# Kernel optimization log

Measured on AMD Instinct MI355X. Metric: run time of the kernel, lower is better.

The kernel has to match this reference:

```python
import jax, jax.numpy as jnp
import numpy as np

B, N, DIN, DOUT, H, DH, DC, NL, L = 8, 256, 64, 64, 8, 8, 64, 32, 2
SCALE = DH ** -0.5  # out_dim-per-head scaling used by both attention variants


def _ln(x, g, b):
    m = jnp.mean(x, -1, keepdims=True)
    v = jnp.mean((x - m) ** 2, -1, keepdims=True)
    return (x - m) * jax.lax.rsqrt(v + 1e-5) * g + b


def _cross_attn(x, ctx, mask_b, wq, wkv, wo, bo):
    # CrossAttentionLayer: standard softmax attention with clamp(-5,5)
    b, n, _ = x.shape
    m = ctx.shape[1]
    q = (x @ wq).reshape(b, n, H, DH).transpose(0, 2, 1, 3)
    k, v = jnp.split(ctx @ wkv, 2, axis=-1)
    k = k.reshape(b, m, H, DH).transpose(0, 2, 1, 3)
    v = v.reshape(b, m, H, DH).transpose(0, 2, 1, 3)
    sim = jnp.einsum('bhid,bhjd->bhij', q, k) * SCALE
    if mask_b is not None:
        sim = jnp.where(mask_b[:, None, None, :], sim, -jnp.finfo(sim.dtype).max)
    sim = jnp.clip(sim, -5.0, 5.0)
    attn = jax.nn.softmax(sim, axis=-1)
    out = jnp.einsum('bhij,bhjd->bhid', attn, v)
    out = out.transpose(0, 2, 1, 3).reshape(b, n, H * DH)
    return out @ wo + bo


def _mha_edge(p, e, k_RW, mask, wq, wk, we, wv):
    # GraphiT MultiHeadAttentionLayer with edge features + k_RW attention PE
    Q = (p @ wq).reshape(B, N, H, DH)
    K = (p @ wk).reshape(B, N, H, DH) * SCALE
    V = (p @ wv).reshape(B, N, H, DH).transpose(0, 2, 1, 3)  # [B,H,N,d]
    E = (e @ we).reshape(B, N, N, H, DH)
    scores = jnp.einsum('bihk,bjhk,bijhk->bhij', Q, K, E)
    scores = jnp.exp(scores - jnp.max(scores, axis=(-2, -1), keepdims=True))
    scores = scores * mask[:, None, :, None] * mask[:, None, None, :]
    scores = scores * k_RW
    denom = jnp.clip(jnp.sum(scores, -1, keepdims=True), 1e-6, None)
    out = jnp.einsum('bhij,bhjd->bhid', scores, V) / denom
    return out.transpose(0, 2, 1, 3).reshape(B, N, H * DH)


def setup_inputs() -> dict:
    key = jax.random.key(0)
    ks = jax.random.split(key, 32)
    rn = lambda k, s: jax.random.normal(k, s, dtype=jnp.float32)
    inp = {
        'h': rn(ks[0], (B, N, DIN)),
        'p': rn(ks[1], (B, N, DIN)),
        'e': rn(ks[2], (B, N, N, DIN)),
        'k_RW': jax.random.uniform(ks[3], (B, 1, N, N), dtype=jnp.float32),
        'queries': rn(ks[4], (B, NL, DC)),
        'mask': jnp.ones((B, N), dtype=jnp.float32),
        # attention_p (MultiHeadAttentionLayer) weights
        'wq_p': rn(ks[5], (DIN, H * DH)) * 0.05,
        'wk_p': rn(ks[6], (DIN, H * DH)) * 0.05,
        'we_p': rn(ks[7], (DIN, H * DH)) * 0.05,
        'wv_p': rn(ks[8], (DIN, H * DH)) * 0.05,
        'wo_p': rn(ks[9], (DOUT, DOUT)) * 0.05,
        # cross_attention_h (queries attend to nodes)
        'cq_wq': rn(ks[10], (DC, H * DH)) * 0.05,
        'cq_wkv': rn(ks[11], (DIN, 2 * H * DH)) * 0.05,
        'cq_wo': rn(ks[12], (H * DH, DC)) * 0.05,
        'cq_bo': jnp.zeros((DC,), dtype=jnp.float32),
        # L_cross latent self-attention layers (stacked)
        'sa_wq': rn(ks[13], (L, DC, H * DH)) * 0.05,
        'sa_wkv': rn(ks[14], (L, DC, 2 * H * DH)) * 0.05,
        'sa_wo': rn(ks[15], (L, H * DH, DC)) * 0.05,
        'sa_bo': jnp.zeros((L, DC), dtype=jnp.float32),
        # O_queries, norms, FFN
        'oq_w': rn(ks[16], (DC, DC)) * 0.05,
        'ln1_g': jnp.ones((DC,), dtype=jnp.float32),
        'ln1_b': jnp.zeros((DC,), dtype=jnp.float32),
        'ffn_w1': rn(ks[17], (DC, 2 * DC)) * 0.05,
        'ffn_w2': rn(ks[18], (2 * DC, DC)) * 0.05,
        'ln2_g': jnp.ones((DC,), dtype=jnp.float32),
        'ln2_b': jnp.zeros((DC,), dtype=jnp.float32),
    }
    return inp


def reference(h, p, e, k_RW, queries, mask,
              wq_p, wk_p, we_p, wv_p, wo_p,
              cq_wq, cq_wkv, cq_wo, cq_bo,
              sa_wq, sa_wkv, sa_wo, sa_bo,
              oq_w, ln1_g, ln1_b, ffn_w1, ffn_w2, ln2_g, ln2_b):
    # forward_p: update positional encoding via edge-modulated attention
    p_attn = _mha_edge(p, e, k_RW, mask, wq_p, wk_p, we_p, wv_p)
    p_new = p + jnp.tanh(p_attn @ wo_p)  # residual, no dropout (eval)
    # combine node features with updated PE (use_node_pe='sum')
    h_c = h + p_new
    mask_b = mask > 0.5
    # perceiver cross-attention: latents attend to nodes
    q = queries + _cross_attn(queries, h_c, mask_b, cq_wq, cq_wkv, cq_wo, cq_bo)
    # L_cross latent self-attention blocks with residual
    for i in range(L):
        q = q + _cross_attn(q, q, None, sa_wq[i], sa_wkv[i], sa_wo[i], sa_bo[i])
    # O_queries projection + layer norm
    q = _ln(q @ oq_w, ln1_g, ln1_b)
    # feed-forward block on queries
    ff = jax.nn.relu(q @ ffn_w1) @ ffn_w2
    q = _ln(q + ff, ln2_g, ln2_b)
    return q
```

## Files before the change

kernel.cpp:

```cpp
#include <hip/hip_runtime.h>
#include <hip/hip_bf16.h>
#include <math.h>

typedef __bf16 bf16x8 __attribute__((ext_vector_type(8)));
typedef float floatx4 __attribute__((ext_vector_type(4)));

#define ATT_SCALE 0.35355339059327373f

__device__ __forceinline__ __bf16 f2b(float x) { return (__bf16)x; }

__global__ void k_proj(const float* __restrict__ p, const float* __restrict__ quer,
                       const float* __restrict__ wq, const float* __restrict__ wk,
                       const float* __restrict__ wv, const float* __restrict__ cq_wq,
                       float* __restrict__ Q, float* __restrict__ Ks,
                       float* __restrict__ V, float* __restrict__ q1) {
  int blk = blockIdx.x, t = threadIdx.x;
  __shared__ float xr[64];
  if (blk < 2048) {
    xr[t] = p[blk * 64 + t];
    __syncthreads();
    float aq = 0.f, ak = 0.f, av = 0.f;
    for (int c = 0; c < 64; c++) {
      float x = xr[c];
      aq += x * wq[c * 64 + t];
      ak += x * wk[c * 64 + t];
      av += x * wv[c * 64 + t];
    }
    Q[blk * 64 + t] = aq;
    Ks[blk * 64 + t] = ak * ATT_SCALE;
    V[blk * 64 + t] = av;
  } else {
    int r = blk - 2048;
    xr[t] = quer[r * 64 + t];
    __syncthreads();
    float a = 0.f;
    for (int c = 0; c < 64; c++) a += xr[c] * cq_wq[c * 64 + t];
    q1[r * 64 + t] = a;
  }
}

__global__ __launch_bounds__(256) void k_edge(
    const float* __restrict__ e, const float* __restrict__ we,
    const float* __restrict__ krw, const float* __restrict__ mask,
    const float* __restrict__ hin, const float* __restrict__ pin,
    const float* __restrict__ wo, const float* __restrict__ cq_wkv,
    const float* __restrict__ Q, const float* __restrict__ Ks,
    const float* __restrict__ V, float* __restrict__ Kc, float* __restrict__ Vc) {
  int bi = blockIdx.x;
  int b = bi >> 8;
  int t = threadIdx.x;
  int w = t >> 6, l = t & 63;
  int l15 = l & 15, quad = l >> 4, half8 = (l >> 3) & 1, d = l & 7;

  bf16x8 wfrag[4][2];
  for (int nt = 0; nt < 4; nt++)
    for (int kc = 0; kc < 2; kc++)
      for (int jj = 0; jj < 8; jj++)
        wfrag[nt][kc][jj] = f2b(we[(kc * 32 + quad * 8 + jj) * 64 + nt * 16 + l15]);

  float qv[4];
  for (int nt = 0; nt < 4; nt++) qv[nt] = Q[bi * 64 + nt * 16 + l15];
  float mi = mask[bi];

  float aout[4] = {0.f, 0.f, 0.f, 0.f};
  float aden[4] = {0.f, 0.f, 0.f, 0.f};

  for (int mt = 0; mt < 4; mt++) {
    int j0 = w * 64 + mt * 16;
    const float* ep = e + ((long)bi * 256 + j0 + l15) * 64 + quad * 8;
    float4 ea = *reinterpret_cast<const float4*>(ep);
    float4 eb4 = *reinterpret_cast<const float4*>(ep + 4);
    float4 ec = *reinterpret_cast<const float4*>(ep + 32);
    float4 ed4 = *reinterpret_cast<const float4*>(ep + 36);
    bf16x8 a0, a1;
    a0[0] = f2b(ea.x); a0[1] = f2b(ea.y); a0[2] = f2b(ea.z); a0[3] = f2b(ea.w);
    a0[4] = f2b(eb4.x); a0[5] = f2b(eb4.y); a0[6] = f2b(eb4.z); a0[7] = f2b(eb4.w);
    a1[0] = f2b(ec.x); a1[1] = f2b(ec.y); a1[2] = f2b(ec.z); a1[3] = f2b(ec.w);
    a1[4] = f2b(ed4.x); a1[5] = f2b(ed4.y); a1[6] = f2b(ed4.z); a1[7] = f2b(ed4.w);

    int jr0 = j0 + quad * 4;
    float krw_r[4], mj_r[4];
    for (int r = 0; r < 4; r++) {
      krw_r[r] = krw[(long)bi * 256 + jr0 + r];
      mj_r[r] = mask[b * 256 + jr0 + r];
    }
    for (int nt = 0; nt < 4; nt++) {
      floatx4 acc = {0.f, 0.f, 0.f, 0.f};
      acc = __builtin_amdgcn_mfma_f32_16x16x32_bf16(a0, wfrag[nt][0], acc, 0, 0, 0);
      acc = __builtin_amdgcn_mfma_f32_16x16x32_bf16(a1, wfrag[nt][1], acc, 0, 0, 0);
      int hk = nt * 16 + l15;
      int hbase = hk & 56;
      for (int r = 0; r < 4; r++) {
        int jr = jr0 + r;
        float s = acc[r] * qv[nt] * Ks[(b * 256 + jr) * 64 + hk];
        s += __shfl_xor(s, 1);
        s += __shfl_xor(s, 2);
        s += __shfl_xor(s, 4);
        float wg = __expf(s) * krw_r[r] * mj_r[r];
        aden[nt] += wg;
        aout[nt] += wg * V[(b * 256 + jr) * 64 + hbase + d];
      }
    }
  }
  for (int nt = 0; nt < 4; nt++) {
    float o = aout[nt], dn = aden[nt];
    o += __shfl_xor(o, 16); o += __shfl_xor(o, 32);
    dn += __shfl_xor(dn, 16); dn += __shfl_xor(dn, 32);
    aout[nt] = o; aden[nt] = dn;
  }

  __shared__ float red[4][64];
  __shared__ float redden[4][8];
  __shared__ float pav[64];
  __shared__ float hcl[64];
  if (l < 16) {
    for (int nt = 0; nt < 4; nt++) {
      int head = nt * 2 + half8;
      red[w][head * 8 + d] = aout[nt];
      if (d == 0) redden[w][head] = aden[nt];
    }
  }
  __syncthreads();
  if (t < 64) {
    int head = t >> 3;
    float num = red[0][t] + red[1][t] + red[2][t] + red[3][t];
    float den = redden[0][head] + redden[1][head] + redden[2][head] + redden[3][head];
    num *= mi;
    den = fmaxf(den * mi, 1e-6f);
    pav[t] = num / den;
  }
  __syncthreads();
  if (t < 64) {
    float a = 0.f;
    for (int c = 0; c < 64; c++) a += pav[c] * wo[c * 64 + t];
    hcl[t] = hin[bi * 64 + t] + pin[bi * 64 + t] + tanhf(a);
  }
  __syncthreads();
  if (t < 128) {
    float a = 0.f;
    for (int c = 0; c < 64; c++) a += hcl[c] * cq_wkv[c * 128 + t];
    if (t < 64) Kc[bi * 64 + t] = a;
    else        Vc[bi * 64 + t - 64] = a;
  }
}

__global__ void k_cross(const float* __restrict__ q1, const float* __restrict__ Kc,
                        const float* __restrict__ Vc, const float* __restrict__ mask,
                        float* __restrict__ oc) {
  int bh = blockIdx.x, b = bh >> 3, h = bh & 7;
  int t = threadIdx.x, r = t >> 3, g = t & 7;
  __shared__ float qL[32][8];
  qL[r][g] = q1[(b * 32 + r) * 64 + h * 8 + g];
  __syncthreads();
  float num[8] = {0.f, 0.f, 0.f, 0.f, 0.f, 0.f, 0.f, 0.f};
  float den = 0.f;
  for (int jj = 0; jj < 32; jj++) {
    int j = jj * 8 + g;
    const float* kp = Kc + (b * 256 + j) * 64 + h * 8;
    float s = 0.f;
    for (int dd = 0; dd < 8; dd++) s += qL[r][dd] * kp[dd];
    s *= ATT_SCALE;
    float mj = mask[b * 256 + j];
    s = (mj > 0.5f) ? s : -1e30f;
    s = fminf(fmaxf(s, -5.f), 5.f);
    float ex = __expf(s);
    den += ex;
    const float* vp = Vc + (b * 256 + j) * 64 + h * 8;
    for (int dd = 0; dd < 8; dd++) num[dd] += ex * vp[dd];
  }
  den += __shfl_xor(den, 1); den += __shfl_xor(den, 2); den += __shfl_xor(den, 4);
  for (int dd = 0; dd < 8; dd++) {
    float v = num[dd];
    v += __shfl_xor(v, 1); v += __shfl_xor(v, 2); v += __shfl_xor(v, 4);
    num[dd] = v;
  }
  oc[(b * 32 + r) * 64 + h * 8 + g] = num[g] / den;
}

__global__ void k_projqkv(const float* __restrict__ attn_in, const float* __restrict__ Wo,
                          const float* __restrict__ bo, const float* __restrict__ residp,
                          const float* __restrict__ wql, const float* __restrict__ wkvl,
                          float* __restrict__ q_out, float* __restrict__ qq,
                          float* __restrict__ kvb) {
  int r = blockIdx.x, t = threadIdx.x;
  __shared__ float oL[64];
  __shared__ float qL[64];
  oL[t] = attn_in[r * 64 + t];
  __syncthreads();
  float a = 0.f;
  for (int c = 0; c < 64; c++) a += oL[c] * Wo[c * 64 + t];
  float qvv = residp[r * 64 + t] + a + bo[t];
  q_out[r * 64 + t] = qvv;
  qL[t] = qvv;
  __syncthreads();
  float aq = 0.f, ak = 0.f, av = 0.f;
  for (int c = 0; c < 64; c++) {
    float x = qL[c];
    aq += x * wql[c * 64 + t];
    ak += x * wkvl[c * 128 + t];
    av += x * wkvl[c * 128 + 64 + t];
  }
  qq[r * 64 + t] = aq;
  kvb[r * 128 + t] = ak;
  kvb[r * 128 + 64 + t] = av;
}

__global__ void k_sattn(const float* __restrict__ qq, const float* __restrict__ kvb,
                        float* __restrict__ os) {
  int bh = blockIdx.x, b = bh >> 3, h = bh & 7;
  int t = threadIdx.x, r = t >> 3, g = t & 7;
  __shared__ float qL[32][8];
  qL[r][g] = qq[(b * 32 + r) * 64 + h * 8 + g];
  __syncthreads();
  float num[8] = {0.f, 0.f, 0.f, 0.f, 0.f, 0.f, 0.f, 0.f};
  float den = 0.f;
  for (int jj = 0; jj < 4; jj++) {
    int j = jj * 8 + g;
    const float* kp = kvb + (b * 32 + j) * 128 + h * 8;
    float s = 0.f;
    for (int dd = 0; dd < 8; dd++) s += qL[r][dd] * kp[dd];
    s *= ATT_SCALE;
    s = fminf(fmaxf(s, -5.f), 5.f);
    float ex = __expf(s);
    den += ex;
    for (int dd = 0; dd < 8; dd++) num[dd] += ex * kp[64 + dd];
  }
  den += __shfl_xor(den, 1); den += __shfl_xor(den, 2); den += __shfl_xor(den, 4);
  for (int dd = 0; dd < 8; dd++) {
    float v = num[dd];
    v += __shfl_xor(v, 1); v += __shfl_xor(v, 2); v += __shfl_xor(v, 4);
    num[dd] = v;
  }
  os[(b * 32 + r) * 64 + h * 8 + g] = num[g] / den;
}

__global__ void k_final(const float* __restrict__ os, const float* __restrict__ Wo,
                        const float* __restrict__ bo, const float* __restrict__ qprev,
                        const float* __restrict__ oqw, const float* __restrict__ g1,
                        const float* __restrict__ b1, const float* __restrict__ w1,
                        const float* __restrict__ w2, const float* __restrict__ g2,
                        const float* __restrict__ b2v, float* __restrict__ out) {
  int r = blockIdx.x, t = threadIdx.x;
  __shared__ float oL[64];
  __shared__ float q2L[64];
  __shared__ float yL[64];
  __shared__ float hhs[128];
  oL[t] = os[r * 64 + t];
  __syncthreads();
  float a = 0.f;
  for (int c = 0; c < 64; c++) a += oL[c] * Wo[c * 64 + t];
  float q2 = qprev[r * 64 + t] + a + bo[t];
  q2L[t] = q2;
  __syncthreads();
  float x = 0.f;
  for (int c = 0; c < 64; c++) x += q2L[c] * oqw[c * 64 + t];
  float m = x;
  for (int off = 1; off < 64; off <<= 1) m += __shfl_xor(m, off);
  m *= (1.f / 64.f);
  float dv = x - m, vv = dv * dv;
  for (int off = 1; off < 64; off <<= 1) vv += __shfl_xor(vv, off);
  vv *= (1.f / 64.f);
  float y = dv * rsqrtf(vv + 1e-5f) * g1[t] + b1[t];
  yL[t] = y;
  __syncthreads();
  float h1 = 0.f, h2 = 0.f;
  for (int c = 0; c < 64; c++) {
    float xx = yL[c];
    h1 += xx * w1[c * 128 + t];
    h2 += xx * w1[c * 128 + 64 + t];
  }
  hhs[t] = fmaxf(h1, 0.f);
  hhs[t + 64] = fmaxf(h2, 0.f);
  __syncthreads();
  float ff = 0.f;
  for (int c = 0; c < 128; c++) ff += hhs[c] * w2[c * 64 + t];
  float z = y + ff;
  float m2 = z;
  for (int off = 1; off < 64; off <<= 1) m2 += __shfl_xor(m2, off);
  m2 *= (1.f / 64.f);
  float dz = z - m2, v2 = dz * dz;
  for (int off = 1; off < 64; off <<= 1) v2 += __shfl_xor(v2, off);
  v2 *= (1.f / 64.f);
  float z2 = dz * rsqrtf(v2 + 1e-5f) * g2[t] + b2v[t];
  out[r * 64 + t] = z2;
}

extern "C" void kernel_launch(void* const* d_in, const int* in_sizes, int n_in,
                              void* d_out, int out_size, void* d_ws, size_t ws_size,
                              hipStream_t stream) {
  const float* h_in   = (const float*)d_in[0];
  const float* p_in   = (const float*)d_in[1];
  const float* e_in   = (const float*)d_in[2];
  const float* krw    = (const float*)d_in[3];
  const float* quer   = (const float*)d_in[4];
  const float* mask   = (const float*)d_in[5];
  const float* wq_p   = (const float*)d_in[6];
  const float* wk_p   = (const float*)d_in[7];
  const float* we_p   = (const float*)d_in[8];
  const float* wv_p   = (const float*)d_in[9];
  const float* wo_p   = (const float*)d_in[10];
  const float* cq_wq  = (const float*)d_in[11];
  const float* cq_wkv = (const float*)d_in[12];
  const float* cq_wo  = (const float*)d_in[13];
  const float* cq_bo  = (const float*)d_in[14];
  const float* sa_wq  = (const float*)d_in[15];
  const float* sa_wkv = (const float*)d_in[16];
  const float* sa_wo  = (const float*)d_in[17];
  const float* sa_bo  = (const float*)d_in[18];
  const float* oq_w   = (const float*)d_in[19];
  const float* ln1_g  = (const float*)d_in[20];
  const float* ln1_b  = (const float*)d_in[21];
  const float* ffn_w1 = (const float*)d_in[22];
  const float* ffn_w2 = (const float*)d_in[23];
  const float* ln2_g  = (const float*)d_in[24];
  const float* ln2_b  = (const float*)d_in[25];

  float* ws = (float*)d_ws;
  float* Q   = ws;
  float* Ks  = Q + 131072;
  float* V   = Ks + 131072;
  float* q1  = V + 131072;
  float* Kc  = q1 + 16384;
  float* Vc  = Kc + 131072;
  float* oc  = Vc + 131072;
  float* q0  = oc + 16384;
  float* qq  = q0 + 16384;
  float* kvb = qq + 16384;
  float* osa = kvb + 32768;
  float* qc1 = osa + 16384;

  k_proj<<<2304, 64, 0, stream>>>(p_in, quer, wq_p, wk_p, wv_p, cq_wq, Q, Ks, V, q1);
  k_edge<<<2048, 256, 0, stream>>>(e_in, we_p, krw, mask, h_in, p_in, wo_p, cq_wkv,
                                   Q, Ks, V, Kc, Vc);
  k_cross<<<64, 256, 0, stream>>>(q1, Kc, Vc, mask, oc);
  k_projqkv<<<256, 64, 0, stream>>>(oc, cq_wo, cq_bo, quer,
                                    sa_wq, sa_wkv, q0, qq, kvb);
  k_sattn<<<64, 256, 0, stream>>>(qq, kvb, osa);
  k_projqkv<<<256, 64, 0, stream>>>(osa, sa_wo, sa_bo, q0,
                                    sa_wq + 4096, sa_wkv + 8192, qc1, qq, kvb);
  k_sattn<<<64, 256, 0, stream>>>(qq, kvb, osa);
  k_final<<<256, 64, 0, stream>>>(osa, sa_wo + 4096, sa_bo + 64, qc1, oq_w,
                                  ln1_g, ln1_b, ffn_w1, ffn_w2, ln2_g, ln2_b,
                                  (float*)d_out);
}
```

Baseline: 311.2 us.

## Transpose edge MFMA layout, prefetch edge tiles, fuse latent attention stages

The edge kernel swaps the MFMA operand order so each lane holds four head-dim outputs for a single key j. The per-row score reduction becomes one shuffle plus vector loads of Ks, V and Q, and the next edge tile is prefetched in registers. The downstream latent pipeline fuses cross-attention, output projection and next QKV projection into single kernels: k_crossf, k_sattnf, and k_finalf with K/V staged in LDS. This removes three kernel launches and intermediate round trips. The cost is more register pressure in k_edge and fewer, heavier blocks in the fused tail kernels.

Result: slower. 322.1 us (+3.5%).

```diff
diff --git a/kernel.cpp b/kernel.cpp
--- a/kernel.cpp
+++ b/kernel.cpp
@@ -50,7 +50,9 @@
   int b = bi >> 8;
   int t = threadIdx.x;
   int w = t >> 6, l = t & 63;
-  int l15 = l & 15, quad = l >> 4, half8 = (l >> 3) & 1, d = l & 7;
+  int l15 = l & 15, quad = l >> 4;
+  int hsel = quad >> 1;
+  int par = quad & 1;
 
   bf16x8 wfrag[4][2];
   for (int nt = 0; nt < 4; nt++)
@@ -58,66 +60,90 @@
       for (int jj = 0; jj < 8; jj++)
         wfrag[nt][kc][jj] = f2b(we[(kc * 32 + quad * 8 + jj) * 64 + nt * 16 + l15]);
 
-  float qv[4];
-  for (int nt = 0; nt < 4; nt++) qv[nt] = Q[bi * 64 + nt * 16 + l15];
+  float4 qv[4];
+#pragma unroll
+  for (int nt = 0; nt < 4; nt++)
+    qv[nt] = *(const float4*)(Q + bi * 64 + nt * 16 + quad * 4);
+
   float mi = mask[bi];
 
-  float aout[4] = {0.f, 0.f, 0.f, 0.f};
+  float aout[4][4];
   float aden[4] = {0.f, 0.f, 0.f, 0.f};
-
-  for (int mt = 0; mt < 4; mt++) {
-    int j0 = w * 64 + mt * 16;
-    const float* ep = e + ((long)bi * 256 + j0 + l15) * 64 + quad * 8;
-    float4 ea = *reinterpret_cast<const float4*>(ep);
-    float4 eb4 = *reinterpret_cast<const float4*>(ep + 4);
-    float4 ec = *reinterpret_cast<const float4*>(ep + 32);
-    float4 ed4 = *reinterpret_cast<const float4*>(ep + 36);
+#pragma unroll
+  for (int nt = 0; nt < 4; nt++)
+#pragma unroll
+    for (int d = 0; d < 4; d++) aout[nt][d] = 0.f;
+
+  const float* ebase = e + ((long)bi * 256 + w * 64 + l15) * 64 + quad * 8;
+  float4 c0 = *(const float4*)(ebase);
+  float4 c1 = *(const float4*)(ebase + 4);
+  float4 c2 = *(const float4*)(ebase + 32);
+  float4 c3 = *(const float4*)(ebase + 36);
+
+  for (int jt = 0; jt < 4; jt++) {
+    float4 n0, n1, n2, n3;
+    if (jt < 3) {
+      const float* np = ebase + (jt + 1) * 1024;
+      n0 = *(const float4*)(np);
+      n1 = *(const float4*)(np + 4);
+      n2 = *(const float4*)(np + 32);
+      n3 = *(const float4*)(np + 36);
+    }
+    int j = w * 64 + jt * 16 + l15;
     bf16x8 a0, a1;
-    a0[0] = f2b(ea.x); a0[1] = f2b(ea.y); a0[2] = f2b(ea.z); a0[3] = f2b(ea.w);
-    a0[4] = f2b(eb4.x); a0[5] = f2b(eb4.y); a0[6] = f2b(eb4.z); a0[7] = f2b(eb4.w);
-    a1[0] = f2b(ec.x); a1[1] = f2b(ec.y); a1[2] = f2b(ec.z); a1[3] = f2b(ec.w);
-    a1[4] = f2b(ed4.x); a1[5] = f2b(ed4.y); a1[6] = f2b(ed4.z); a1[7] = f2b(ed4.w);
-
-    int jr0 = j0 + quad * 4;
-    float krw_r[4], mj_r[4];
-    for (int r = 0; r < 4; r++) {
-      krw_r[r] = krw[(long)bi * 256 + jr0 + r];
-      mj_r[r] = mask[b * 256 + jr0 + r];
-    }
+    a0[0] = f2b(c0.x); a0[1] = f2b(c0.y); a0[2] = f2b(c0.z); a0[3] = f2b(c0.w);
+    a0[4] = f2b(c1.x); a0[5] = f2b(c1.y); a0[6] = f2b(c1.z); a0[7] = f2b(c1.w);
+    a1[0] = f2b(c2.x); a1[1] = f2b(c2.y); a1[2] = f2b(c2.z); a1[3] = f2b(c2.w);
+    a1[4] = f2b(c3.x); a1[5] = f2b(c3.y); a1[6] = f2b(c3.z); a1[7] = f2b(c3.w);
+
+    float kwm = krw[(long)bi * 256 + j] * mask[b * 256 + j];
+    const float* ksrow = Ks + ((long)(b * 256 + j)) * 64 + quad * 4;
+    const float* vrow = V + ((long)(b * 256 + j)) * 64 + hsel * 8 + par * 4;
+
+#pragma unroll
     for (int nt = 0; nt < 4; nt++) {
       floatx4 acc = {0.f, 0.f, 0.f, 0.f};
-      acc = __builtin_amdgcn_mfma_f32_16x16x32_bf16(a0, wfrag[nt][0], acc, 0, 0, 0);
-      acc = __builtin_amdgcn_mfma_f32_16x16x32_bf16(a1, wfrag[nt][1], acc, 0, 0, 0);
-      int hk = nt * 16 + l15;
-      int hbase = hk & 56;
-      for (int r = 0; r < 4; r++) {
-        int jr = jr0 + r;
-        float s = acc[r] * qv[nt] * Ks[(b * 256 + jr) * 64 + hk];
-        s += __shfl_xor(s, 1);
-        s += __shfl_xor(s, 2);
-        s += __shfl_xor(s, 4);
-        float wg = __expf(s) * krw_r[r] * mj_r[r];
-        aden[nt] += wg;
-        aout[nt] += wg * V[(b * 256 + jr) * 64 + hbase + d];
-      }
-    }
-  }
+      acc = __builtin_amdgcn_mfma_f32_16x16x32_bf16(wfrag[nt][0], a0, acc, 0, 0, 0);
+      acc = __builtin_amdgcn_mfma_f32_16x16x32_bf16(wfrag[nt][1], a1, acc, 0, 0, 0);
+      float4 kf = *(const float4*)(ksrow + nt * 16);
+      float s = acc[0] * kf.x * qv[nt].x + acc[1] * kf.y * qv[nt].y +
+                acc[2] * kf.z * qv[nt].z + acc[3] * kf.w * qv[nt].w;
+      s += __shfl_xor(s, 16);
+      float wg = __expf(s) * kwm;
+      aden[nt] += wg;
+      float4 va = *(const float4*)(vrow + nt * 16);
+      aout[nt][0] += wg * va.x; aout[nt][1] += wg * va.y;
+      aout[nt][2] += wg * va.z; aout[nt][3] += wg * va.w;
+    }
+    if (jt < 3) { c0 = n0; c1 = n1; c2 = n2; c3 = n3; }
+  }
+
+#pragma unroll
   for (int nt = 0; nt < 4; nt++) {
-    float o = aout[nt], dn = aden[nt];
-    o += __shfl_xor(o, 16); o += __shfl_xor(o, 32);
-    dn += __shfl_xor(dn, 16); dn += __shfl_xor(dn, 32);
-    aout[nt] = o; aden[nt] = dn;
+    float dn = aden[nt];
+    dn += __shfl_xor(dn, 1); dn += __shfl_xor(dn, 2);
+    dn += __shfl_xor(dn, 4); dn += __shfl_xor(dn, 8);
+    aden[nt] = dn;
+#pragma unroll
+    for (int d = 0; d < 4; d++) {
+      float o = aout[nt][d];
+      o += __shfl_xor(o, 1); o += __shfl_xor(o, 2);
+      o += __shfl_xor(o, 4); o += __shfl_xor(o, 8);
+      aout[nt][d] = o;
+    }
   }
 
   __shared__ float red[4][64];
   __shared__ float redden[4][8];
   __shared__ float pav[64];
   __shared__ float hcl[64];
-  if (l < 16) {
+  if (l15 == 0) {
+#pragma unroll
     for (int nt = 0; nt < 4; nt++) {
-      int head = nt * 2 + half8;
-      red[w][head * 8 + d] = aout[nt];
-      if (d == 0) redden[w][head] = aden[nt];
+      int head = nt * 2 + hsel;
+#pragma unroll
+      for (int d = 0; d < 4; d++) red[w][head * 8 + par * 4 + d] = aout[nt][d];
+      if (par == 0) redden[w][head] = aden[nt];
     }
   }
   __syncthreads();
@@ -144,145 +170,255 @@
   }
 }
 
-__global__ void k_cross(const float* __restrict__ q1, const float* __restrict__ Kc,
-                        const float* __restrict__ Vc, const float* __restrict__ mask,
-                        float* __restrict__ oc) {
-  int bh = blockIdx.x, b = bh >> 3, h = bh & 7;
-  int t = threadIdx.x, r = t >> 3, g = t & 7;
-  __shared__ float qL[32][8];
-  qL[r][g] = q1[(b * 32 + r) * 64 + h * 8 + g];
+__global__ __launch_bounds__(256) void k_crossf(
+    const float* __restrict__ q1, const float* __restrict__ Kc,
+    const float* __restrict__ Vc, const float* __restrict__ mask,
+    const float* __restrict__ quer, const float* __restrict__ cq_wo,
+    const float* __restrict__ cq_bo, const float* __restrict__ wq0,
+    const float* __restrict__ wkv0, float* __restrict__ q0g,
+    float* __restrict__ qqg, float* __restrict__ kvg) {
+  int blk = blockIdx.x, b = blk >> 3, rg = blk & 7;
+  int t = threadIdx.x, rr = t >> 6, l = t & 63, h = l >> 3, g = l & 7;
+  int gr = b * 32 + rg * 4 + rr;
+  __shared__ float ocs[4][64];
+  __shared__ float q0s[4][64];
+
+  {
+    const float* qp = q1 + gr * 64 + h * 8;
+    float4 qa = *(const float4*)qp, qb = *(const float4*)(qp + 4);
+    float num[8] = {0.f, 0.f, 0.f, 0.f, 0.f, 0.f, 0.f, 0.f};
+    float den = 0.f;
+#pragma unroll 4
+    for (int jj = 0; jj < 32; jj++) {
+      int j = jj * 8 + g;
+      const float* kp = Kc + (b * 256 + j) * 64 + h * 8;
+      float4 ka = *(const float4*)kp, kb = *(const float4*)(kp + 4);
+      float s = qa.x * ka.x + qa.y * ka.y + qa.z * ka.z + qa.w * ka.w +
+                qb.x * kb.x + qb.y * kb.y + qb.z * kb.z + qb.w * kb.w;
+      s *= ATT_SCALE;
+      float mj = mask[b * 256 + j];
+      s = (mj > 0.5f) ? s : -1e30f;
+      s = fminf(fmaxf(s, -5.f), 5.f);
+      float ex = __expf(s);
+      den += ex;
+      const float* vp = Vc + (b * 256 + j) * 64 + h * 8;
+      float4 va = *(const float4*)vp, vb = *(const float4*)(vp + 4);
+      num[0] += ex * va.x; num[1] += ex * va.y;
+      num[2] += ex * va.z; num[3] += ex * va.w;
+      num[4] += ex * vb.x; num[5] += ex * vb.y;
+      num[6] += ex * vb.z; num[7] += ex * vb.w;
+    }
+    den += __shfl_xor(den, 1); den += __shfl_xor(den, 2); den += __shfl_xor(den, 4);
+#pragma unroll
+    for (int d = 0; d < 8; d++) {
+      float v = num[d];
+      v += __shfl_xor(v, 1); v += __shfl_xor(v, 2); v += __shfl_xor(v, 4);
+      num[d] = v;
+    }
+    float sel = num[0];
+#pragma unroll
+    for (int d = 1; d < 8; d++) sel = (g == d) ? num[d] : sel;
+    ocs[rr][h * 8 + g] = sel / den;
+  }
+
+  int c = l;
+  {
+    float acc = quer[gr * 64 + c] + cq_bo[c];
+    for (int k = 0; k < 64; k++) acc += ocs[rr][k] * cq_wo[k * 64 + c];
+    q0g[gr * 64 + c] = acc;
+    q0s[rr][c] = acc;
+  }
+  {
+    float aq = 0.f, ak = 0.f, av = 0.f;
+    for (int k = 0; k < 64; k++) {
+      float x = q0s[rr][k];
+      aq += x * wq0[k * 64 + c];
+      ak += x * wkv0[k * 128 + c];
+      av += x * wkv0[k * 128 + 64 + c];
+    }
+    qqg[gr * 64 + c] = aq;
+    kvg[gr * 128 + c] = ak;
+    kvg[gr * 128 + 64 + c] = av;
+  }
+}
+
+__global__ __launch_bounds__(256) void k_sattnf(
+    const float* __restrict__ qq, const float* __restrict__ kv,
+    const float* __restrict__ resid, const float* __restrict__ wo,
+    const float* __restrict__ bo, const float* __restrict__ wq2,
+    const float* __restrict__ wkv2, float* __restrict__ q_out,
+    float* __restrict__ qq2, float* __restrict__ kv2) {
+  int blk = blockIdx.x, b = blk >> 3, rg = blk & 7;
+  int t = threadIdx.x, rr = t >> 6, l = t & 63, h = l >> 3, g = l & 7;
+  int gr = b * 32 + rg * 4 + rr;
+  __shared__ float KVs[32][128];
+  __shared__ float ocs[4][64];
+  __shared__ float q2s[4][64];
+
+  const float4* s4 = (const float4*)(kv + b * 4096);
+  float4* d4 = (float4*)&KVs[0][0];
+#pragma unroll
+  for (int i = 0; i < 4; i++) d4[i * 256 + t] = s4[i * 256 + t];
+
+  const float* qp = qq + gr * 64 + h * 8;
+  float4 qa = *(const float4*)qp, qb = *(const float4*)(qp + 4);
   __syncthreads();
-  float num[8] = {0.f, 0.f, 0.f, 0.f, 0.f, 0.f, 0.f, 0.f};
-  float den = 0.f;
-  for (int jj = 0; jj < 32; jj++) {
-    int j = jj * 8 + g;
-    const float* kp = Kc + (b * 256 + j) * 64 + h * 8;
-    float s = 0.f;
-    for (int dd = 0; dd < 8; dd++) s += qL[r][dd] * kp[dd];
-    s *= ATT_SCALE;
-    float mj = mask[b * 256 + j];
-    s = (mj > 0.5f) ? s : -1e30f;
-    s = fminf(fmaxf(s, -5.f), 5.f);
-    float ex = __expf(s);
-    den += ex;
-    const float* vp = Vc + (b * 256 + j) * 64 + h * 8;
-    for (int dd = 0; dd < 8; dd++) num[dd] += ex * vp[dd];
-  }
-  den += __shfl_xor(den, 1); den += __shfl_xor(den, 2); den += __shfl_xor(den, 4);
-  for (int dd = 0; dd < 8; dd++) {
-    float v = num[dd];
-    v += __shfl_xor(v, 1); v += __shfl_xor(v, 2); v += __shfl_xor(v, 4);
-    num[dd] = v;
-  }
-  oc[(b * 32 + r) * 64 + h * 8 + g] = num[g] / den;
-}
-
-__global__ void k_projqkv(const float* __restrict__ attn_in, const float* __restrict__ Wo,
-                          const float* __restrict__ bo, const float* __restrict__ residp,
-                          const float* __restrict__ wql, const float* __restrict__ wkvl,
-                          float* __restrict__ q_out, float* __restrict__ qq,
-                          float* __restrict__ kvb) {
-  int r = blockIdx.x, t = threadIdx.x;
-  __shared__ float oL[64];
-  __shared__ float qL[64];
-  oL[t] = attn_in[r * 64 + t];
+
+  {
+    float num[8] = {0.f, 0.f, 0.f, 0.f, 0.f, 0.f, 0.f, 0.f};
+    float den = 0.f;
+#pragma unroll
+    for (int jj = 0; jj < 4; jj++) {
+      int j = jj * 8 + g;
+      float4 ka = *(const float4*)&KVs[j][h * 8];
+      float4 kb = *(const float4*)&KVs[j][h * 8 + 4];
+      float s = qa.x * ka.x + qa.y * ka.y + qa.z * ka.z + qa.w * ka.w +
+                qb.x * kb.x + qb.y * kb.y + qb.z * kb.z + qb.w * kb.w;
+      s *= ATT_SCALE;
+      s = fminf(fmaxf(s, -5.f), 5.f);
+      float ex = __expf(s);
+      den += ex;
+      float4 va = *(const float4*)&KVs[j][64 + h * 8];
+      float4 vb = *(const float4*)&KVs[j][64 + h * 8 + 4];
+      num[0] += ex * va.x; num[1] += ex * va.y;
+      num[2] += ex * va.z; num[3] += ex * va.w;
+      num[4] += ex * vb.x; num[5] += ex * vb.y;
+      num[6] += ex * vb.z; num[7] += ex * vb.w;
+    }
+    den += __shfl_xor(den, 1); den += __shfl_xor(den, 2); den += __shfl_xor(den, 4);
+#pragma unroll
+    for (int d = 0; d < 8; d++) {
+      float v = num[d];
+      v += __shfl_xor(v, 1); v += __shfl_xor(v, 2); v += __shfl_xor(v, 4);
+      num[d] = v;
+    }
+    float sel = num[0];
+#pragma unroll
+    for (int d = 1; d < 8; d++) sel = (g == d) ? num[d] : sel;
+    ocs[rr][h * 8 + g] = sel / den;
+  }
+
+  int c = l;
+  {
+    float acc = resid[gr * 64 + c] + bo[c];
+    for (int k = 0; k < 64; k++) acc += ocs[rr][k] * wo[k * 64 + c];
+    q_out[gr * 64 + c] = acc;
+    q2s[rr][c] = acc;
+  }
+  {
+    float aq = 0.f, ak = 0.f, av = 0.f;
+    for (int k = 0; k < 64; k++) {
+      float x = q2s[rr][k];
+      aq += x * wq2[k * 64 + c];
+      ak += x * wkv2[k * 128 + c];
+      av += x * wkv2[k * 128 + 64 + c];
+    }
+    qq2[gr * 64 + c] = aq;
+    kv2[gr * 128 + c] = ak;
+    kv2[gr * 128 + 64 + c] = av;
+  }
+}
+
+__global__ __launch_bounds__(256) void k_finalf(
+    const float* __restrict__ qq, const float* __restrict__ kv,
+    const float* __restrict__ resid, const float* __restrict__ wo,
+    const float* __restrict__ bo, const float* __restrict__ oqw,
+    const float* __restrict__ g1, const float* __restrict__ b1,
+    const float* __restrict__ w1, const float* __restrict__ w2,
+    const float* __restrict__ g2, const float* __restrict__ b2v,
+    float* __restrict__ out) {
+  int blk = blockIdx.x, b = blk >> 3, rg = blk & 7;
+  int t = threadIdx.x, rr = t >> 6, l = t & 63, h = l >> 3, g = l & 7;
+  int gr = b * 32 + rg * 4 + rr;
+  __shared__ float KVs[32][128];
+  __shared__ float ocs[4][64];
+  __shared__ float xs[4][64];
+  __shared__ float hs[4][128];
+
+  const float4* s4 = (const float4*)(kv + b * 4096);
+  float4* d4 = (float4*)&KVs[0][0];
+#pragma unroll
+  for (int i = 0; i < 4; i++) d4[i * 256 + t] = s4[i * 256 + t];
+
+  const float* qp = qq + gr * 64 + h * 8;
+  float4 qa = *(const float4*)qp, qb = *(const float4*)(qp + 4);
   __syncthreads();
-  float a = 0.f;
-  for (int c = 0; c < 64; c++) a += oL[c] * Wo[c * 64 + t];
-  float qvv = residp[r * 64 + t] + a + bo[t];
-  q_out[r * 64 + t] = qvv;
-  qL[t] = qvv;
-  __syncthreads();
-  float aq = 0.f, ak = 0.f, av = 0.f;
-  for (int c = 0; c < 64; c++) {
-    float x = qL[c];
-    aq += x * wql[c * 64 + t];
-    ak += x * wkvl[c * 128 + t];
-    av += x * wkvl[c * 128 + 64 + t];
-  }
-  qq[r * 64 + t] = aq;
-  kvb[r * 128 + t] = ak;
-  kvb[r * 128 + 64 + t] = av;
-}
-
-__global__ void k_sattn(const float* __restrict__ qq, const float* __restrict__ kvb,
-                        float* __restrict__ os) {
-  int bh = blockIdx.x, b = bh >> 3, h = bh & 7;
-  int t = threadIdx.x, r = t >> 3, g = t & 7;
-  __shared__ float qL[32][8];
-  qL[r][g] = qq[(b * 32 + r) * 64 + h * 8 + g];
-  __syncthreads();
-  float num[8] = {0.f, 0.f, 0.f, 0.f, 0.f, 0.f, 0.f, 0.f};
-  float den = 0.f;
-  for (int jj = 0; jj < 4; jj++) {
-    int j = jj * 8 + g;
-    const float* kp = kvb + (b * 32 + j) * 128 + h * 8;
-    float s = 0.f;
-    for (int dd = 0; dd < 8; dd++) s += qL[r][dd] * kp[dd];
-    s *= ATT_SCALE;
-    s = fminf(fmaxf(s, -5.f), 5.f);
-    float ex = __expf(s);
-    den += ex;
-    for (int dd = 0; dd < 8; dd++) num[dd] += ex * kp[64 + dd];
-  }
-  den += __shfl_xor(den, 1); den += __shfl_xor(den, 2); den += __shfl_xor(den, 4);
-  for (int dd = 0; dd < 8; dd++) {
-    float v = num[dd];
-    v += __shfl_xor(v, 1); v += __shfl_xor(v, 2); v += __shfl_xor(v, 4);
-    num[dd] = v;
-  }
-  os[(b * 32 + r) * 64 + h * 8 + g] = num[g] / den;
-}
-
-__global__ void k_final(const float* __restrict__ os, const float* __restrict__ Wo,
-                        const float* __restrict__ bo, const float* __restrict__ qprev,
-                        const float* __restrict__ oqw, const float* __restrict__ g1,
-                        const float* __restrict__ b1, const float* __restrict__ w1,
-                        const float* __restrict__ w2, const float* __restrict__ g2,
-                        const float* __restrict__ b2v, float* __restrict__ out) {
-  int r = blockIdx.x, t = threadIdx.x;
-  __shared__ float oL[64];
-  __shared__ float q2L[64];
-  __shared__ float yL[64];
-  __shared__ float hhs[128];
-  oL[t] = os[r * 64 + t];
-  __syncthreads();
-  float a = 0.f;
-  for (int c = 0; c < 64; c++) a += oL[c] * Wo[c * 64 + t];
-  float q2 = qprev[r * 64 + t] + a + bo[t];
-  q2L[t] = q2;
-  __syncthreads();
-  float x = 0.f;
-  for (int c = 0; c < 64; c++) x += q2L[c] * oqw[c * 64 + t];
-  float m = x;
-  for (int off = 1; off < 64; off <<= 1) m += __shfl_xor(m, off);
-  m *= (1.f / 64.f);
-  float dv = x - m, vv = dv * dv;
-  for (int off = 1; off < 64; off <<= 1) vv += __shfl_xor(vv, off);
-  vv *= (1.f / 64.f);
-  float y = dv * rsqrtf(vv + 1e-5f) * g1[t] + b1[t];
-  yL[t] = y;
-  __syncthreads();
-  float h1 = 0.f, h2 = 0.f;
-  for (int c = 0; c < 64; c++) {
-    float xx = yL[c];
-    h1 += xx * w1[c * 128 + t];
-    h2 += xx * w1[c * 128 + 64 + t];
-  }
-  hhs[t] = fmaxf(h1, 0.f);
-  hhs[t + 64] = fmaxf(h2, 0.f);
-  __syncthreads();
-  float ff = 0.f;
-  for (int c = 0; c < 128; c++) ff += hhs[c] * w2[c * 64 + t];
-  float z = y + ff;
-  float m2 = z;
-  for (int off = 1; off < 64; off <<= 1) m2 += __shfl_xor(m2, off);
-  m2 *= (1.f / 64.f);
-  float dz = z - m2, v2 = dz * dz;
-  for (int off = 1; off < 64; off <<= 1) v2 += __shfl_xor(v2, off);
-  v2 *= (1.f / 64.f);
-  float z2 = dz * rsqrtf(v2 + 1e-5f) * g2[t] + b2v[t];
-  out[r * 64 + t] = z2;
+
+  {
+    float num[8] = {0.f, 0.f, 0.f, 0.f, 0.f, 0.f, 0.f, 0.f};
+    float den = 0.f;
+#pragma unroll
+    for (int jj = 0; jj < 4; jj++) {
+      int j = jj * 8 + g;
+      float4 ka = *(const float4*)&KVs[j][h * 8];
+      float4 kb = *(const float4*)&KVs[j][h * 8 + 4];
+      float s = qa.x * ka.x + qa.y * ka.y + qa.z * ka.z + qa.w * ka.w +
+                qb.x * kb.x + qb.y * kb.y + qb.z * kb.z + qb.w * kb.w;
+      s *= ATT_SCALE;
+      s = fminf(fmaxf(s, -5.f), 5.f);
+      float ex = __expf(s);
+      den += ex;
+      float4 va = *(const float4*)&KVs[j][64 + h * 8];
+      float4 vb = *(const float4*)&KVs[j][64 + h * 8 + 4];
+      num[0] += ex * va.x; num[1] += ex * va.y;
+      num[2] += ex * va.z; num[3] += ex * va.w;
+      num[4] += ex * vb.x; num[5] += ex * vb.y;
+      num[6] += ex * vb.z; num[7] += ex * vb.w;
+    }
+    den += __shfl_xor(den, 1); den += __shfl_xor(den, 2); den += __shfl_xor(den, 4);
+#pragma unroll
+    for (int d = 0; d < 8; d++) {
+      float v = num[d];
+      v += __shfl_xor(v, 1); v += __shfl_xor(v, 2); v += __shfl_xor(v, 4);
+      num[d] = v;
+    }
+    float sel = num[0];
+#pragma unroll
+    for (int d = 1; d < 8; d++) sel = (g == d) ? num[d] : sel;
+    ocs[rr][h * 8 + g] = sel / den;
+  }
+
+  int c = l;
+  float y;
+  {
+    float acc = resid[gr * 64 + c] + bo[c];
+    for (int k = 0; k < 64; k++) acc += ocs[rr][k] * wo[k * 64 + c];
+    xs[rr][c] = acc;
+  }
+  {
+    float x = 0.f;
+    for (int k = 0; k < 64; k++) x += xs[rr][k] * oqw[k * 64 + c];
+    float m = x;
+    for (int off = 1; off < 64; off <<= 1) m += __shfl_xor(m, off);
+    m *= (1.f / 64.f);
+    float dv = x - m, vv = dv * dv;
+    for (int off = 1; off < 64; off <<= 1) vv += __shfl_xor(vv, off);
+    vv *= (1.f / 64.f);
+    y = dv * rsqrtf(vv + 1e-5f) * g1[c] + b1[c];
+    xs[rr][c] = y;
+  }
+  {
+    float h1 = 0.f, h2 = 0.f;
+    for (int k = 0; k < 64; k++) {
+      float xx = xs[rr][k];
+      h1 += xx * w1[k * 128 + c];
+      h2 += xx * w1[k * 128 + 64 + c];
+    }
+    hs[rr][c] = fmaxf(h1, 0.f);
+    hs[rr][64 + c] = fmaxf(h2, 0.f);
+  }
+  {
+    float ff = 0.f;
+    for (int k = 0; k < 128; k++) ff += hs[rr][k] * w2[k * 64 + c];
+    float z = y + ff;
+    float m2 = z;
+    for (int off = 1; off < 64; off <<= 1) m2 += __shfl_xor(m2, off);
+    m2 *= (1.f / 64.f);
+    float dz = z - m2, v2 = dz * dz;
+    for (int off = 1; off < 64; off <<= 1) v2 += __shfl_xor(v2, off);
+    v2 *= (1.f / 64.f);
+    out[gr * 64 + c] = dz * rsqrtf(v2 + 1e-5f) * g2[c] + b2v[c];
+  }
 }
 
 extern "C" void kernel_launch(void* const* d_in, const int* in_sizes, int n_in,
@@ -322,24 +458,21 @@
   float* q1  = V + 131072;
   float* Kc  = q1 + 16384;
   float* Vc  = Kc + 131072;
-  float* oc  = Vc + 131072;
-  float* q0  = oc + 16384;
-  float* qq  = q0 + 16384;
-  float* kvb = qq + 16384;
-  float* osa = kvb + 32768;
-  float* qc1 = osa + 16384;
+  float* q0  = Vc + 131072;
+  float* qc1 = q0 + 16384;
+  float* qqA = qc1 + 16384;
+  float* qqB = qqA + 16384;
+  float* kvA = qqB + 16384;
+  float* kvB = kvA + 32768;
 
   k_proj<<<2304, 64, 0, stream>>>(p_in, quer, wq_p, wk_p, wv_p, cq_wq, Q, Ks, V, q1);
   k_edge<<<2048, 256, 0, stream>>>(e_in, we_p, krw, mask, h_in, p_in, wo_p, cq_wkv,
                                    Q, Ks, V, Kc, Vc);
-  k_cross<<<64, 256, 0, stream>>>(q1, Kc, Vc, mask, oc);
-  k_projqkv<<<256, 64, 0, stream>>>(oc, cq_wo, cq_bo, quer,
-                                    sa_wq, sa_wkv, q0, qq, kvb);
-  k_sattn<<<64, 256, 0, stream>>>(qq, kvb, osa);
-  k_projqkv<<<256, 64, 0, stream>>>(osa, sa_wo, sa_bo, q0,
-                                    sa_wq + 4096, sa_wkv + 8192, qc1, qq, kvb);
-  k_sattn<<<64, 256, 0, stream>>>(qq, kvb, osa);
-  k_final<<<256, 64, 0, stream>>>(osa, sa_wo + 4096, sa_bo + 64, qc1, oq_w,
-                                  ln1_g, ln1_b, ffn_w1, ffn_w2, ln2_g, ln2_b,
-                                  (float*)d_out);
-}
+  k_crossf<<<64, 256, 0, stream>>>(q1, Kc, Vc, mask, quer, cq_wo, cq_bo,
+                                   sa_wq, sa_wkv, q0, qqA, kvA);
+  k_sattnf<<<64, 256, 0, stream>>>(qqA, kvA, q0, sa_wo, sa_bo,
+                                   sa_wq + 4096, sa_wkv + 8192, qc1, qqB, kvB);
+  k_finalf<<<64, 256, 0, stream>>>(qqB, kvB, qc1, sa_wo + 4096, sa_bo + 64, oq_w,
+                                   ln1_g, ln1_b, ffn_w1, ffn_w2, ln2_g, ln2_b,
+                                   (float*)d_out);
+}
```
